# Kernel tuning notes

Measured on AMD Instinct MI355X. Metric: run time of the kernel, lower is better.

Reference implementation:

```python
import jax, jax.numpy as jnp
import numpy as np

D = 256          # input_dim (node embedding dim)
ATT_TIMES = 2
ATT_NUM = 2
DIN = D * ATT_NUM  # NTN input dim = 512
F = 16           # feature_map_dim


def setup_inputs() -> dict:
    key = jax.random.key(0)
    ks = jax.random.split(key, 10)
    x1 = jax.random.normal(ks[0], (120000, D), dtype=jnp.float32)
    x2 = jax.random.normal(ks[1], (100000, D), dtype=jnp.float32)
    # attention weight (glorot)
    W0 = jax.random.normal(ks[2], (D, D), dtype=jnp.float32) * (2.0 / (D + D)) ** 0.5
    # NTN params
    V = jax.random.normal(ks[3], (F, 2 * DIN), dtype=jnp.float32) * (2.0 / (F + 2 * DIN)) ** 0.5
    W = jax.random.normal(ks[4], (F, DIN, DIN), dtype=jnp.float32) * (2.0 / (DIN + DIN)) ** 0.5
    b = jax.random.normal(ks[5], (F,), dtype=jnp.float32)
    # projection MLP 16->8->4->2->1, torch Linear weights are (out, in)
    P0 = jax.random.normal(ks[6], (8, 16), dtype=jnp.float32) * (2.0 / (8 + 16)) ** 0.5
    P1 = jax.random.normal(ks[7], (4, 8), dtype=jnp.float32) * (2.0 / (4 + 8)) ** 0.5
    P2 = jax.random.normal(ks[8], (2, 4), dtype=jnp.float32) * (2.0 / (2 + 4)) ** 0.5
    P3 = jax.random.normal(ks[9], (1, 2), dtype=jnp.float32) * (2.0 / (1 + 2)) ** 0.5
    return {"x1": x1, "x2": x2, "W0": W0, "V": V, "W": W, "b": b,
            "P0": P0, "P1": P1, "P2": P2, "P3": P3}


def _attention(x, W0):
    # x: (N, D) -> (1, D*ATT_NUM) graph embedding.
    outs = []
    for _ in range(ATT_NUM):  # 'dot' style: same params each head (eye W), kept for faithfulness
        cur = x
        out = None
        for _ in range(ATT_TIMES):
            temp = jnp.mean(cur, axis=0, keepdims=True)          # (1, D)
            h_avg = jnp.tanh(temp @ W0)                          # att_weight=True
            att = jax.nn.sigmoid(cur @ h_avg.T)                  # (N, 1), W=eye in 'dot' style
            out = att.T @ cur                                    # (1, D)
            cur = cur * att
        outs.append(out)
    return jnp.concatenate(outs, axis=1)                         # (1, DIN)


def _ntn(g1, g2, V, W, b):
    # g1, g2: (1, DIN). Fused bilinear over all F feature maps.
    concat = jnp.concatenate([g1, g2], axis=1)                   # (1, 2*DIN)
    v_term = concat @ V.T                                        # (1, F)
    w_term = jnp.einsum('nd,fde,me->nf', g1, W, g2)              # (1, F)
    return jax.nn.sigmoid(v_term + w_term + b)                   # inneract = sigmoid


def reference(x1, x2, W0, V, W, b, P0, P1, P2, P3):
    g1 = _attention(x1, W0)
    g2 = _attention(x2, W0)
    x = _ntn(g1, g2, V, W, b)                                    # (1, F), branch 'an'
    for P in (P0, P1, P2, P3):                                   # Linear(no bias) + Sigmoid
        x = jax.nn.sigmoid(x @ P.T)
    return x                                                     # (1, 1)
```

## Files before the change

kernel.cpp:

```cpp
#include <hip/hip_runtime.h>
#include <math.h>

#define DD 256
#define REPS 8

#define OFF_SUMREP 0
#define OFF_H1P    4096
#define OFF_S1REP  4608
#define OFF_H2P    8704
#define OFF_OREP   9216
#define OFF_WTREP  13824
#define WS_FLOATS  13952
#define MIRROR_OFF_BYTES 65536

typedef float    f32x4 __attribute__((ext_vector_type(4)));
typedef _Float16 f16x4 __attribute__((ext_vector_type(4)));

__device__ __forceinline__ float sigmoidf_(float x) { return 1.0f / (1.0f + __expf(-x)); }
__device__ __forceinline__ float dot4(f32x4 a, f32x4 b) {
    return a.x * b.x + a.y * b.y + a.z * b.z + a.w * b.w;
}
__device__ __forceinline__ f32x4 tanh4(f32x4 a) {
    f32x4 r; r.x = tanhf(a.x); r.y = tanhf(a.y); r.z = tanhf(a.z); r.w = tanhf(a.w);
    return r;
}
__device__ __forceinline__ float wave_sum(float v) {
#pragma unroll
    for (int off = 32; off; off >>= 1) v += __shfl_xor(v, off, 64);
    return v;
}
__device__ __forceinline__ f32x4 ld4(const f32x4* p, size_t i) { return p[i]; }
__device__ __forceinline__ f32x4 ld4(const f16x4* p, size_t i) {
    return __builtin_convertvector(p[i], f32x4);
}

__global__ void k_zero(float* __restrict__ ws) {
    int i = blockIdx.x * 256 + threadIdx.x;
    if (i < WS_FLOATS) ws[i] = 0.0f;
}

__device__ __forceinline__ void block_reduce_atomic(f32x4 acc, int t, float* dst_base,
                                                    f32x4* lds) {
    lds[t] = acc;
    __syncthreads();
    if (t < 64) {
        f32x4 s = lds[t] + lds[t + 64] + lds[t + 128] + lds[t + 192];
        float* dst = dst_base + t * 4;
        atomicAdd(dst + 0, s.x); atomicAdd(dst + 1, s.y);
        atomicAdd(dst + 2, s.z); atomicAdd(dst + 3, s.w);
    }
}

template<bool WM>
__global__ void __launch_bounds__(256, 4)
k_mean_t(const f32x4* __restrict__ x1, const f32x4* __restrict__ x2,
         f16x4* __restrict__ m1, f16x4* __restrict__ m2,
         int N1, int N2, float* __restrict__ ws) {
    int b = blockIdx.x, t = threadIdx.x;
    int inp = b >> 10, bl = b & 1023;
    const f32x4* x = inp ? x2 : x1;
    f16x4* mm = inp ? m2 : m1;
    int N = inp ? N2 : N1;
    int chunk = (N + 1023) >> 10;
    int start = bl * chunk, end = min(start + chunk, N);
    int lane = t & 63, w = t >> 6;
    f32x4 a0 = {0.f, 0.f, 0.f, 0.f}, a1 = a0;
    int r = start + w;
    for (; r + 12 < end; r += 16) {
        size_t i0 = (size_t)r * 64 + lane;
        f32x4 v0 = x[i0], v1 = x[i0 + 256], v2 = x[i0 + 512], v3 = x[i0 + 768];
        if (WM) {
            mm[i0]       = __builtin_convertvector(v0, f16x4);
            mm[i0 + 256] = __builtin_convertvector(v1, f16x4);
            mm[i0 + 512] = __builtin_convertvector(v2, f16x4);
            mm[i0 + 768] = __builtin_convertvector(v3, f16x4);
        }
        a0 += v0 + v1; a1 += v2 + v3;
    }
    for (; r < end; r += 4) {
        size_t i0 = (size_t)r * 64 + lane;
        f32x4 v = x[i0];
        if (WM) mm[i0] = __builtin_convertvector(v, f16x4);
        a0 += v;
    }
    a0 += a1;
    __shared__ f32x4 lds[256];
    block_reduce_atomic(a0, t, ws + OFF_SUMREP + inp * (REPS * 256) + (bl & (REPS - 1)) * 256, lds);
}

__global__ void k_hpart(const float* __restrict__ W0, float* __restrict__ ws,
                        int srcOff, int dstOff, int N1, int N2) {
    int inp = blockIdx.x >> 4, g = blockIdx.x & 15;
    int t = threadIdx.x;
    __shared__ float temp[16];
    if (t < 16) {
        const float* src = ws + srcOff + inp * (REPS * 256) + g * 16 + t;
        float s = 0.f;
#pragma unroll
        for (int r = 0; r < REPS; r++) s += src[r * 256];
        temp[t] = s * (1.0f / (float)(inp ? N2 : N1));
    }
    __syncthreads();
    float p = 0.f;
#pragma unroll
    for (int j = 0; j < 16; j++) p += temp[j] * W0[(g * 16 + j) * 256 + t];
    atomicAdd(ws + dstOff + inp * 256 + t, p);
}

template<typename T>
__global__ void __launch_bounds__(256, 4)
k_att1_t(const T* __restrict__ b1, const T* __restrict__ b2,
         int N1, int N2, float* __restrict__ ws) {
    int b = blockIdx.x, t = threadIdx.x;
    int inp = b >> 10, bl = b & 1023;
    const T* x = inp ? b2 : b1;
    int N = inp ? N2 : N1;
    int chunk = (N + 1023) >> 10;
    int start = bl * chunk, end = min(start + chunk, N);
    int lane = t & 63, w = t >> 6;
    f32x4 h1 = tanh4(((const f32x4*)(ws + OFF_H1P + inp * 256))[lane]);
    f32x4 acc = {0.f, 0.f, 0.f, 0.f};
    int r = start + w;
    for (; r + 12 < end; r += 16) {
        size_t i0 = (size_t)r * 64 + lane;
        f32x4 v0 = ld4(x, i0), v1 = ld4(x, i0 + 256), v2 = ld4(x, i0 + 512), v3 = ld4(x, i0 + 768);
        float d0 = dot4(v0, h1), d1 = dot4(v1, h1), d2 = dot4(v2, h1), d3 = dot4(v3, h1);
#pragma unroll
        for (int off = 32; off; off >>= 1) {
            d0 += __shfl_xor(d0, off, 64); d1 += __shfl_xor(d1, off, 64);
            d2 += __shfl_xor(d2, off, 64); d3 += __shfl_xor(d3, off, 64);
        }
        acc += sigmoidf_(d0) * v0 + sigmoidf_(d1) * v1;
        acc += sigmoidf_(d2) * v2 + sigmoidf_(d3) * v3;
    }
    for (; r < end; r += 4) {
        f32x4 v = ld4(x, (size_t)r * 64 + lane);
        acc += sigmoidf_(wave_sum(dot4(v, h1))) * v;
    }
    __shared__ f32x4 lds[256];
    block_reduce_atomic(acc, t, ws + OFF_S1REP + inp * (REPS * 256) + (bl & (REPS - 1)) * 256, lds);
}

template<typename T>
__global__ void __launch_bounds__(256, 4)
k_att2_t(const T* __restrict__ b1, const T* __restrict__ b2,
         int N1, int N2, float* __restrict__ ws) {
    int b = blockIdx.x, t = threadIdx.x;
    int inp = b >> 10, bl = b & 1023;
    const T* x = inp ? b2 : b1;
    int N = inp ? N2 : N1;
    int chunk = (N + 1023) >> 10;
    int start = bl * chunk, end = min(start + chunk, N);
    int lane = t & 63, w = t >> 6;
    f32x4 h1 = tanh4(((const f32x4*)(ws + OFF_H1P + inp * 256))[lane]);
    f32x4 h2 = tanh4(((const f32x4*)(ws + OFF_H2P + inp * 256))[lane]);
    f32x4 acc = {0.f, 0.f, 0.f, 0.f};
    int r = start + w;
    for (; r + 4 < end; r += 8) {
        size_t i0 = (size_t)r * 64 + lane;
        f32x4 v0 = ld4(x, i0), v1 = ld4(x, i0 + 256);
        float d0 = dot4(v0, h1), d1 = dot4(v1, h1);
        float e0 = dot4(v0, h2), e1 = dot4(v1, h2);
#pragma unroll
        for (int off = 32; off; off >>= 1) {
            d0 += __shfl_xor(d0, off, 64); e0 += __shfl_xor(e0, off, 64);
            d1 += __shfl_xor(d1, off, 64); e1 += __shfl_xor(e1, off, 64);
        }
        float a0 = sigmoidf_(d0), a1 = sigmoidf_(d1);
        acc += (a0 * sigmoidf_(a0 * e0)) * v0 + (a1 * sigmoidf_(a1 * e1)) * v1;
    }
    for (; r < end; r += 4) {
        f32x4 v = ld4(x, (size_t)r * 64 + lane);
        float d = dot4(v, h1), e = dot4(v, h2);
#pragma unroll
        for (int off = 32; off; off >>= 1) {
            d += __shfl_xor(d, off, 64); e += __shfl_xor(e, off, 64);
        }
        float a1 = sigmoidf_(d);
        acc += (a1 * sigmoidf_(a1 * e)) * v;
    }
    __shared__ f32x4 lds[256];
    block_reduce_atomic(acc, t, ws + OFF_OREP + inp * (REPS * 256) + (bl & (REPS - 1)) * 256, lds);
}

__global__ void __launch_bounds__(256, 4)
k_ntn(const float* __restrict__ W, float* __restrict__ ws) {
    __shared__ __align__(16) float o_l[512];
    int b = blockIdx.x, t = threadIdx.x;
    {
        float s0 = 0.f, s1 = 0.f;
#pragma unroll
        for (int r2 = 0; r2 < REPS; r2++) {
            s0 += ws[OFF_OREP + r2 * 256 + t];
            s1 += ws[OFF_OREP + REPS * 256 + r2 * 256 + t];
        }
        o_l[t] = s0; o_l[256 + t] = s1;
    }
    __syncthreads();
    int lane = t & 63, w = t >> 6;
    f32x4 o2f = ((const f32x4*)(o_l + 256))[lane];
    int g = b * 4 + w;
    const f32x4* W4 = (const f32x4*)W;
    float wt[4];
    int fidx[4];
#pragma unroll
    for (int u = 0; u < 4; u++) {
        int row = g + u * 2048;
        const f32x4* q = W4 + (size_t)row * 128 + lane;
        float p = wave_sum(dot4(q[0] + q[64], o2f));
        wt[u] = o_l[row & 255] * p;
        fidx[u] = row >> 9;
    }
    if (lane == 0) {
        float* dst = ws + OFF_WTREP + (b & (REPS - 1)) * 16;
#pragma unroll
        for (int u = 0; u < 4; u++) atomicAdd(dst + fidx[u], wt[u]);
    }
}

__global__ void k_final(const float* __restrict__ V, const float* __restrict__ bb,
                        const float* __restrict__ P0, const float* __restrict__ P1,
                        const float* __restrict__ P2, const float* __restrict__ P3,
                        float* __restrict__ ws, float* __restrict__ out) {
    int t = threadIdx.x;
    __shared__ float o_l[512];
    {
        float s0 = 0.f, s1 = 0.f;
#pragma unroll
        for (int r2 = 0; r2 < REPS; r2++) {
            s0 += ws[OFF_OREP + r2 * 256 + t];
            s1 += ws[OFF_OREP + REPS * 256 + r2 * 256 + t];
        }
        o_l[t] = s0; o_l[256 + t] = s1;
    }
    __syncthreads();
    int f = t >> 4, j = t & 15;
    float p = 0.f;
    for (int k = j; k < 1024; k += 16) {
        float cv = (k < 512) ? o_l[k & 255] : o_l[256 + (k & 255)];
        p += cv * V[f * 1024 + k];
    }
    __shared__ float red[256];
    __shared__ float sv[16];
    red[t] = p;
    __syncthreads();
    if (t < 16) {
        float v = 0.f;
#pragma unroll
        for (int q = 0; q < 16; q++) v += red[t * 16 + q];
        float wt = 0.f;
#pragma unroll
        for (int r = 0; r < REPS; r++) wt += ws[OFF_WTREP + r * 16 + t];
        sv[t] = sigmoidf_(v + wt + bb[t]);
    }
    __syncthreads();
    if (t == 0) {
        float y0[8], y1[4], y2[2];
#pragma unroll
        for (int i = 0; i < 8; i++) {
            float s = 0.f;
            for (int k = 0; k < 16; k++) s += P0[i * 16 + k] * sv[k];
            y0[i] = sigmoidf_(s);
        }
#pragma unroll
        for (int i = 0; i < 4; i++) {
            float s = 0.f;
            for (int k = 0; k < 8; k++) s += P1[i * 8 + k] * y0[k];
            y1[i] = sigmoidf_(s);
        }
#pragma unroll
        for (int i = 0; i < 2; i++) {
            float s = 0.f;
            for (int k = 0; k < 4; k++) s += P2[i * 4 + k] * y1[k];
            y2[i] = sigmoidf_(s);
        }
        out[0] = sigmoidf_(P3[0] * y2[0] + P3[1] * y2[1]);
    }
}

extern "C" void kernel_launch(void* const* d_in, const int* in_sizes, int n_in,
                              void* d_out, int out_size, void* d_ws, size_t ws_size,
                              hipStream_t stream) {
    const float* x1 = (const float*)d_in[0];
    const float* x2 = (const float*)d_in[1];
    const float* W0 = (const float*)d_in[2];
    const float* V  = (const float*)d_in[3];
    const float* W  = (const float*)d_in[4];
    const float* b  = (const float*)d_in[5];
    const float* P0 = (const float*)d_in[6];
    const float* P1 = (const float*)d_in[7];
    const float* P2 = (const float*)d_in[8];
    const float* P3 = (const float*)d_in[9];
    float* ws  = (float*)d_ws;
    float* out = (float*)d_out;
    int N1 = in_sizes[0] / DD;
    int N2 = in_sizes[1] / DD;

    const f32x4* x1v = (const f32x4*)x1;
    const f32x4* x2v = (const f32x4*)x2;
    f16x4* m1 = (f16x4*)((char*)d_ws + MIRROR_OFF_BYTES);
    f16x4* m2 = m1 + (size_t)N1 * 64;
    size_t need = (size_t)MIRROR_OFF_BYTES + ((size_t)N1 + N2) * DD * sizeof(_Float16);
    bool use_mirror = ws_size >= need;

    k_zero <<<55, 256, 0, stream>>>(ws);
    if (use_mirror) {
        k_mean_t<true>  <<<2048, 256, 0, stream>>>(x1v, x2v, m1, m2, N1, N2, ws);
        k_hpart         <<<32,   256, 0, stream>>>(W0, ws, OFF_SUMREP, OFF_H1P, N1, N2);
        k_att1_t<f16x4> <<<2048, 256, 0, stream>>>(m1, m2, N1, N2, ws);
        k_hpart         <<<32,   256, 0, stream>>>(W0, ws, OFF_S1REP, OFF_H2P, N1, N2);
        k_att2_t<f16x4> <<<2048, 256, 0, stream>>>(m1, m2, N1, N2, ws);
    } else {
        k_mean_t<false> <<<2048, 256, 0, stream>>>(x1v, x2v, nullptr, nullptr, N1, N2, ws);
        k_hpart         <<<32,   256, 0, stream>>>(W0, ws, OFF_SUMREP, OFF_H1P, N1, N2);
        k_att1_t<f32x4> <<<2048, 256, 0, stream>>>(x1v, x2v, N1, N2, ws);
        k_hpart         <<<32,   256, 0, stream>>>(W0, ws, OFF_S1REP, OFF_H2P, N1, N2);
        k_att2_t<f32x4> <<<2048, 256, 0, stream>>>(x1v, x2v, N1, N2, ws);
    }
    k_ntn  <<<512, 256, 0, stream>>>(W, ws);
    k_final<<<1,   256, 0, stream>>>(V, b, P0, P1, P2, P3, ws, out);
}
```

Before: 424.0 us.

## Use grid-stride rows and 8-wide half-wave loads in attention kernels

The row-streaming kernels move from contiguous per-block chunks with 4x unrolling to a grid-stride loop over 1024 blocks. The attention passes now have each half-wave handle one 256-wide row with 8-element vector loads (16-byte fp16 loads from the mirror), so reductions need one fewer shuffle step. Launch-bounds hints and explicit unrolling are dropped. This aims for wider loads and lower shuffle and reduction cost, at the risk of less memory-level parallelism per thread and strided access hurting locality.

```diff
diff --git a/kernel.cpp b/kernel.cpp
--- a/kernel.cpp
+++ b/kernel.cpp
@@ -14,24 +14,20 @@
 #define MIRROR_OFF_BYTES 65536
 
 typedef float    f32x4 __attribute__((ext_vector_type(4)));
+typedef float    f32x8 __attribute__((ext_vector_type(8)));
 typedef _Float16 f16x4 __attribute__((ext_vector_type(4)));
+typedef _Float16 f16x8 __attribute__((ext_vector_type(8)));
 
 __device__ __forceinline__ float sigmoidf_(float x) { return 1.0f / (1.0f + __expf(-x)); }
-__device__ __forceinline__ float dot4(f32x4 a, f32x4 b) {
-    return a.x * b.x + a.y * b.y + a.z * b.z + a.w * b.w;
-}
-__device__ __forceinline__ f32x4 tanh4(f32x4 a) {
-    f32x4 r; r.x = tanhf(a.x); r.y = tanhf(a.y); r.z = tanhf(a.z); r.w = tanhf(a.w);
-    return r;
-}
-__device__ __forceinline__ float wave_sum(float v) {
-#pragma unroll
-    for (int off = 32; off; off >>= 1) v += __shfl_xor(v, off, 64);
-    return v;
-}
-__device__ __forceinline__ f32x4 ld4(const f32x4* p, size_t i) { return p[i]; }
-__device__ __forceinline__ f32x4 ld4(const f16x4* p, size_t i) {
-    return __builtin_convertvector(p[i], f32x4);
+
+__device__ __forceinline__ f32x8 ld8(const f16x8* p, size_t i) {
+    return __builtin_convertvector(p[i], f32x8);
+}
+__device__ __forceinline__ f32x8 ld8(const f32x8* p, size_t i) { return p[i]; }
+
+__device__ __forceinline__ float dot8(f32x8 a, f32x8 b) {
+    f32x8 m = a * b;
+    return ((m[0] + m[4]) + (m[1] + m[5])) + ((m[2] + m[6]) + (m[3] + m[7]));
 }
 
 __global__ void k_zero(float* __restrict__ ws) {
@@ -39,8 +35,8 @@
     if (i < WS_FLOATS) ws[i] = 0.0f;
 }
 
-__device__ __forceinline__ void block_reduce_atomic(f32x4 acc, int t, float* dst_base,
-                                                    f32x4* lds) {
+__device__ __forceinline__ void block_reduce_atomic4(f32x4 acc, int t, float* dst_base) {
+    __shared__ f32x4 lds[256];
     lds[t] = acc;
     __syncthreads();
     if (t < 64) {
@@ -51,41 +47,36 @@
     }
 }
 
+__device__ __forceinline__ void block_reduce_atomic8(f32x8 acc, int t, float* dst_base) {
+    __shared__ f32x8 lds8[256];
+    lds8[t] = acc;
+    __syncthreads();
+    const float* lf = (const float*)lds8;
+    float s = 0.f;
+#pragma unroll
+    for (int slot = 0; slot < 8; slot++) s += lf[slot * 256 + t];
+    atomicAdd(dst_base + t, s);
+}
+
 template<bool WM>
-__global__ void __launch_bounds__(256, 4)
-k_mean_t(const f32x4* __restrict__ x1, const f32x4* __restrict__ x2,
-         f16x4* __restrict__ m1, f16x4* __restrict__ m2,
-         int N1, int N2, float* __restrict__ ws) {
+__global__ void k_mean_t(const f32x4* __restrict__ x1, const f32x4* __restrict__ x2,
+                         f16x4* __restrict__ m1, f16x4* __restrict__ m2,
+                         int N1, int N2, float* __restrict__ ws) {
     int b = blockIdx.x, t = threadIdx.x;
-    int inp = b >> 10, bl = b & 1023;
+    int inp = (b < 512) ? 0 : 1;
+    int bl = inp ? (b - 512) : b;
     const f32x4* x = inp ? x2 : x1;
     f16x4* mm = inp ? m2 : m1;
     int N = inp ? N2 : N1;
-    int chunk = (N + 1023) >> 10;
-    int start = bl * chunk, end = min(start + chunk, N);
-    int lane = t & 63, w = t >> 6;
-    f32x4 a0 = {0.f, 0.f, 0.f, 0.f}, a1 = a0;
-    int r = start + w;
-    for (; r + 12 < end; r += 16) {
-        size_t i0 = (size_t)r * 64 + lane;
-        f32x4 v0 = x[i0], v1 = x[i0 + 256], v2 = x[i0 + 512], v3 = x[i0 + 768];
-        if (WM) {
-            mm[i0]       = __builtin_convertvector(v0, f16x4);
-            mm[i0 + 256] = __builtin_convertvector(v1, f16x4);
-            mm[i0 + 512] = __builtin_convertvector(v2, f16x4);
-            mm[i0 + 768] = __builtin_convertvector(v3, f16x4);
-        }
-        a0 += v0 + v1; a1 += v2 + v3;
-    }
-    for (; r < end; r += 4) {
-        size_t i0 = (size_t)r * 64 + lane;
+    int col4 = t & 63, rg = t >> 6;
+    f32x4 acc = {0.f, 0.f, 0.f, 0.f};
+    for (int r = bl * 4 + rg; r < N; r += 2048) {
+        size_t i0 = (size_t)r * 64 + col4;
         f32x4 v = x[i0];
         if (WM) mm[i0] = __builtin_convertvector(v, f16x4);
-        a0 += v;
-    }
-    a0 += a1;
-    __shared__ f32x4 lds[256];
-    block_reduce_atomic(a0, t, ws + OFF_SUMREP + inp * (REPS * 256) + (bl & (REPS - 1)) * 256, lds);
+        acc += v;
+    }
+    block_reduce_atomic4(acc, t, ws + OFF_SUMREP + inp * (REPS * 256) + (bl & (REPS - 1)) * 256);
 }
 
 __global__ void k_hpart(const float* __restrict__ W0, float* __restrict__ ws,
@@ -108,79 +99,80 @@
 }
 
 template<typename T>
-__global__ void __launch_bounds__(256, 4)
-k_att1_t(const T* __restrict__ b1, const T* __restrict__ b2,
-         int N1, int N2, float* __restrict__ ws) {
+__global__ void k_att1_t(const T* __restrict__ b1, const T* __restrict__ b2,
+                         int N1, int N2, float* __restrict__ ws) {
     int b = blockIdx.x, t = threadIdx.x;
-    int inp = b >> 10, bl = b & 1023;
+    int inp = (b < 512) ? 0 : 1;
+    int bl = inp ? (b - 512) : b;
     const T* x = inp ? b2 : b1;
     int N = inp ? N2 : N1;
-    int chunk = (N + 1023) >> 10;
-    int start = bl * chunk, end = min(start + chunk, N);
     int lane = t & 63, w = t >> 6;
-    f32x4 h1 = tanh4(((const f32x4*)(ws + OFF_H1P + inp * 256))[lane]);
-    f32x4 acc = {0.f, 0.f, 0.f, 0.f};
-    int r = start + w;
-    for (; r + 12 < end; r += 16) {
-        size_t i0 = (size_t)r * 64 + lane;
-        f32x4 v0 = ld4(x, i0), v1 = ld4(x, i0 + 256), v2 = ld4(x, i0 + 512), v3 = ld4(x, i0 + 768);
-        float d0 = dot4(v0, h1), d1 = dot4(v1, h1), d2 = dot4(v2, h1), d3 = dot4(v3, h1);
-#pragma unroll
-        for (int off = 32; off; off >>= 1) {
-            d0 += __shfl_xor(d0, off, 64); d1 += __shfl_xor(d1, off, 64);
-            d2 += __shfl_xor(d2, off, 64); d3 += __shfl_xor(d3, off, 64);
-        }
-        acc += sigmoidf_(d0) * v0 + sigmoidf_(d1) * v1;
-        acc += sigmoidf_(d2) * v2 + sigmoidf_(d3) * v3;
-    }
-    for (; r < end; r += 4) {
-        f32x4 v = ld4(x, (size_t)r * 64 + lane);
-        acc += sigmoidf_(wave_sum(dot4(v, h1))) * v;
-    }
-    __shared__ f32x4 lds[256];
-    block_reduce_atomic(acc, t, ws + OFF_S1REP + inp * (REPS * 256) + (bl & (REPS - 1)) * 256, lds);
+    int half = lane >> 5, l32 = lane & 31;
+    f32x8 h1;
+#pragma unroll
+    for (int j = 0; j < 8; j++) h1[j] = tanhf(ws[OFF_H1P + inp * 256 + l32 * 8 + j]);
+    f32x8 acc = {0.f, 0.f, 0.f, 0.f, 0.f, 0.f, 0.f, 0.f};
+    int wid = bl * 4 + w;
+    int base = wid * 2;
+    for (; base + 1 < N; base += 4096) {
+        int row = base + half;
+        f32x8 v = ld8(x, (size_t)row * 32 + l32);
+        float d = dot8(v, h1);
+#pragma unroll
+        for (int off = 16; off; off >>= 1) d += __shfl_xor(d, off, 64);
+        acc += sigmoidf_(d) * v;
+    }
+    if (base < N && half == 0) {
+        f32x8 v = ld8(x, (size_t)base * 32 + l32);
+        float d = dot8(v, h1);
+#pragma unroll
+        for (int off = 16; off; off >>= 1) d += __shfl_xor(d, off, 64);
+        acc += sigmoidf_(d) * v;
+    }
+    block_reduce_atomic8(acc, t, ws + OFF_S1REP + inp * (REPS * 256) + (bl & (REPS - 1)) * 256);
 }
 
 template<typename T>
-__global__ void __launch_bounds__(256, 4)
-k_att2_t(const T* __restrict__ b1, const T* __restrict__ b2,
-         int N1, int N2, float* __restrict__ ws) {
+__global__ void k_att2_t(const T* __restrict__ b1, const T* __restrict__ b2,
+                         int N1, int N2, float* __restrict__ ws) {
     int b = blockIdx.x, t = threadIdx.x;
-    int inp = b >> 10, bl = b & 1023;
+    int inp = (b < 512) ? 0 : 1;
+    int bl = inp ? (b - 512) : b;
     const T* x = inp ? b2 : b1;
     int N = inp ? N2 : N1;
-    int chunk = (N + 1023) >> 10;
-    int start = bl * chunk, end = min(start + chunk, N);
     int lane = t & 63, w = t >> 6;
-    f32x4 h1 = tanh4(((const f32x4*)(ws + OFF_H1P + inp * 256))[lane]);
-    f32x4 h2 = tanh4(((const f32x4*)(ws + OFF_H2P + inp * 256))[lane]);
-    f32x4 acc = {0.f, 0.f, 0.f, 0.f};
-    int r = start + w;
-    for (; r + 4 < end; r += 8) {
-        size_t i0 = (size_t)r * 64 + lane;
-        f32x4 v0 = ld4(x, i0), v1 = ld4(x, i0 + 256);
-        float d0 = dot4(v0, h1), d1 = dot4(v1, h1);
-        float e0 = dot4(v0, h2), e1 = dot4(v1, h2);
-#pragma unroll
-        for (int off = 32; off; off >>= 1) {
-            d0 += __shfl_xor(d0, off, 64); e0 += __shfl_xor(e0, off, 64);
-            d1 += __shfl_xor(d1, off, 64); e1 += __shfl_xor(e1, off, 64);
-        }
-        float a0 = sigmoidf_(d0), a1 = sigmoidf_(d1);
-        acc += (a0 * sigmoidf_(a0 * e0)) * v0 + (a1 * sigmoidf_(a1 * e1)) * v1;
-    }
-    for (; r < end; r += 4) {
-        f32x4 v = ld4(x, (size_t)r * 64 + lane);
-        float d = dot4(v, h1), e = dot4(v, h2);
-#pragma unroll
-        for (int off = 32; off; off >>= 1) {
+    int half = lane >> 5, l32 = lane & 31;
+    f32x8 h1, h2;
+#pragma unroll
+    for (int j = 0; j < 8; j++) {
+        h1[j] = tanhf(ws[OFF_H1P + inp * 256 + l32 * 8 + j]);
+        h2[j] = tanhf(ws[OFF_H2P + inp * 256 + l32 * 8 + j]);
+    }
+    f32x8 acc = {0.f, 0.f, 0.f, 0.f, 0.f, 0.f, 0.f, 0.f};
+    int wid = bl * 4 + w;
+    int base = wid * 2;
+    for (; base + 1 < N; base += 4096) {
+        int row = base + half;
+        f32x8 v = ld8(x, (size_t)row * 32 + l32);
+        float d = dot8(v, h1), e = dot8(v, h2);
+#pragma unroll
+        for (int off = 16; off; off >>= 1) {
             d += __shfl_xor(d, off, 64); e += __shfl_xor(e, off, 64);
         }
         float a1 = sigmoidf_(d);
         acc += (a1 * sigmoidf_(a1 * e)) * v;
     }
-    __shared__ f32x4 lds[256];
-    block_reduce_atomic(acc, t, ws + OFF_OREP + inp * (REPS * 256) + (bl & (REPS - 1)) * 256, lds);
+    if (base < N && half == 0) {
+        f32x8 v = ld8(x, (size_t)base * 32 + l32);
+        float d = dot8(v, h1), e = dot8(v, h2);
+#pragma unroll
+        for (int off = 16; off; off >>= 1) {
+            d += __shfl_xor(d, off, 64); e += __shfl_xor(e, off, 64);
+        }
+        float a1 = sigmoidf_(d);
+        acc += (a1 * sigmoidf_(a1 * e)) * v;
+    }
+    block_reduce_atomic8(acc, t, ws + OFF_OREP + inp * (REPS * 256) + (bl & (REPS - 1)) * 256);
 }
 
 __global__ void __launch_bounds__(256, 4)
@@ -207,7 +199,10 @@
     for (int u = 0; u < 4; u++) {
         int row = g + u * 2048;
         const f32x4* q = W4 + (size_t)row * 128 + lane;
-        float p = wave_sum(dot4(q[0] + q[64], o2f));
+        f32x4 m = (q[0] + q[64]) * o2f;
+        float p = (m.x + m.y) + (m.z + m.w);
+#pragma unroll
+        for (int off = 32; off; off >>= 1) p += __shfl_xor(p, off, 64);
         wt[u] = o_l[row & 255] * p;
         fidx[u] = row >> 9;
     }
@@ -305,17 +300,17 @@
 
     k_zero <<<55, 256, 0, stream>>>(ws);
     if (use_mirror) {
-        k_mean_t<true>  <<<2048, 256, 0, stream>>>(x1v, x2v, m1, m2, N1, N2, ws);
+        k_mean_t<true>  <<<1024, 256, 0, stream>>>(x1v, x2v, m1, m2, N1, N2, ws);
         k_hpart         <<<32,   256, 0, stream>>>(W0, ws, OFF_SUMREP, OFF_H1P, N1, N2);
-        k_att1_t<f16x4> <<<2048, 256, 0, stream>>>(m1, m2, N1, N2, ws);
+        k_att1_t<f16x8> <<<1024, 256, 0, stream>>>((const f16x8*)m1, (const f16x8*)m2, N1, N2, ws);
         k_hpart         <<<32,   256, 0, stream>>>(W0, ws, OFF_S1REP, OFF_H2P, N1, N2);
-        k_att2_t<f16x4> <<<2048, 256, 0, stream>>>(m1, m2, N1, N2, ws);
+        k_att2_t<f16x8> <<<1024, 256, 0, stream>>>((const f16x8*)m1, (const f16x8*)m2, N1, N2, ws);
     } else {
-        k_mean_t<false> <<<2048, 256, 0, stream>>>(x1v, x2v, nullptr, nullptr, N1, N2, ws);
+        k_mean_t<false> <<<1024, 256, 0, stream>>>(x1v, x2v, nullptr, nullptr, N1, N2, ws);
         k_hpart         <<<32,   256, 0, stream>>>(W0, ws, OFF_SUMREP, OFF_H1P, N1, N2);
-        k_att1_t<f32x4> <<<2048, 256, 0, stream>>>(x1v, x2v, N1, N2, ws);
+        k_att1_t<f32x8> <<<1024, 256, 0, stream>>>((const f32x8*)x1, (const f32x8*)x2, N1, N2, ws);
         k_hpart         <<<32,   256, 0, stream>>>(W0, ws, OFF_S1REP, OFF_H2P, N1, N2);
-        k_att2_t<f32x4> <<<2048, 256, 0, stream>>>(x1v, x2v, N1, N2, ws);
+        k_att2_t<f32x8> <<<1024, 256, 0, stream>>>((const f32x8*)x1, (const f32x8*)x2, N1, N2, ws);
     }
     k_ntn  <<<512, 256, 0, stream>>>(W, ws);
     k_final<<<1,   256, 0, stream>>>(V, b, P0, P1, P2, P3, ws, out);
```

New measurement: 406.2 us. -4.2%, faster.
